# Optimization experiments

Measured on AMD Instinct MI355X. Metric: run time of the kernel, lower is better.

## Reference

```python
import jax, jax.numpy as jnp
import numpy as np

S, B, I, H = 512, 64, 1024, 1024


def setup_inputs() -> dict:
    key = jax.random.key(0)
    ks = jax.random.split(key, 17)
    sI = 1.0 / np.sqrt(I)
    sH = 1.0 / np.sqrt(H)
    d = {"x": jax.random.normal(ks[0], (S, B, I), dtype=jnp.float32)}
    names = ["i", "f", "c", "o"]
    for n, g in enumerate(names):
        d[f"w_x{g}"] = jax.random.uniform(ks[1 + 4 * n], (H, I), jnp.float32, -sI, sI)
        d[f"b_x{g}"] = jax.random.uniform(ks[2 + 4 * n], (H,), jnp.float32, -sI, sI)
        d[f"w_h{g}"] = jax.random.uniform(ks[3 + 4 * n], (H, H), jnp.float32, -sH, sH)
        d[f"b_h{g}"] = jax.random.uniform(ks[4 + 4 * n], (H,), jnp.float32, -sH, sH)
        d[f"b_{g}"] = jnp.zeros((H,), jnp.float32)
    return d


def reference(x, w_xi, b_xi, w_hi, b_hi, b_i,
              w_xf, b_xf, w_hf, b_hf, b_f,
              w_xc, b_xc, w_hc, b_hc, b_c,
              w_xo, b_xo, w_ho, b_ho, b_o):
    seq_len, batch, _ = x.shape
    hid = w_hi.shape[0]
    # Precompute all input-side projections in one big GEMM per gate: [S,B,H].
    # Fold the three bias vectors of each gate (b_x*, b_h*, b_*) in here; math
    # is identical to adding them per step.
    gx_i = jnp.einsum('sbi,hi->sbh', x, w_xi) + (b_xi + b_hi + b_i)
    gx_f = jnp.einsum('sbi,hi->sbh', x, w_xf) + (b_xf + b_hf + b_f)
    gx_c = jnp.einsum('sbi,hi->sbh', x, w_xc) + (b_xc + b_hc + b_c)
    gx_o = jnp.einsum('sbi,hi->sbh', x, w_xo) + (b_xo + b_ho + b_o)

    h0 = jnp.zeros((batch, hid), x.dtype)
    c0 = jnp.zeros((batch, hid), x.dtype)

    def step(carry, gx):
        h, c = carry
        xi, xf, xc, xo = gx
        i_t = jax.nn.sigmoid(xi + h @ w_hi.T)
        f_t = jax.nn.sigmoid(xf + h @ w_hf.T)
        g_t = jnp.tanh(xc + h @ w_hc.T)
        o_t = jax.nn.sigmoid(xo + h @ w_ho.T)
        c = f_t * c + i_t * g_t
        h = o_t * jnp.tanh(c)
        return (h, c), h

    (h, c), outputs = jax.lax.scan(step, (h0, c0), (gx_i, gx_f, gx_c, gx_o))
    return outputs, (h, c)
```

## Files before the change

kernel.cpp:

```cpp
#include <hip/hip_runtime.h>
#include <cstdint>
#include <cstddef>

#define S_LEN 512
#define NB    64
#define NI    1024
#define NH    1024
#define NR    4096
#define NGRP  4
#define WPG   64
#define BPG   16
#define HSLOT 33792
#define FLAGSTRIDE 16

typedef short bf16x8 __attribute__((ext_vector_type(8)));
typedef float f32x4  __attribute__((ext_vector_type(4)));

__device__ __forceinline__ short f2bf(float f) {
  uint32_t u = __float_as_uint(f);
  u += 0x7fff + ((u >> 16) & 1);
  return (short)(u >> 16);
}
__device__ __forceinline__ float bf2f(short s) {
  return __uint_as_float(((uint32_t)(uint16_t)s) << 16);
}
__device__ __forceinline__ void gload16(const void* g, void* l) {
  __builtin_amdgcn_global_load_lds((const __attribute__((address_space(1))) void*)g,
                                   (__attribute__((address_space(3))) void*)l, 16, 0, 0);
}
__device__ __forceinline__ float sigm(float x) { return 1.0f / (1.0f + __expf(-x)); }
__device__ __forceinline__ float tanh_fast(float x) {
  return 2.0f / (1.0f + __expf(-2.0f * x)) - 1.0f;
}

__device__ __forceinline__ void astore32(void* p, uint32_t v) {
  __hip_atomic_store((uint32_t*)p, v, __ATOMIC_RELAXED, __HIP_MEMORY_SCOPE_AGENT);
}
__device__ __forceinline__ uint32_t aload32(const void* p) {
  return __hip_atomic_load((const uint32_t*)p, __ATOMIC_RELAXED, __HIP_MEMORY_SCOPE_AGENT);
}


__global__ __launch_bounds__(256) void k_convert_x(const float* __restrict__ x,
                                                   short* __restrict__ xbf) {
  int tid = blockIdx.x * 256 + threadIdx.x;
  float4 v = ((const float4*)x)[tid];
  short4 o;
  o.x = f2bf(v.x); o.y = f2bf(v.y); o.z = f2bf(v.z); o.w = f2bf(v.w);
  ((short4*)xbf)[tid] = o;
}

struct WPtrs { const float *xi, *xf, *xc, *xo, *hi, *hf, *hc, *ho; };

__global__ __launch_bounds__(256) void k_pack_w(WPtrs w, short* __restrict__ wxcat,
                                                short* __restrict__ whcat) {
  int tid  = blockIdx.x * 256 + threadIdx.x;
  int flat = tid * 4;
  int r = flat >> 10, k = flat & 1023;
  int j = r >> 2, g = r & 3;
  const float* px = (g == 0) ? w.xi : (g == 1) ? w.xf : (g == 2) ? w.xc : w.xo;
  const float* ph = (g == 0) ? w.hi : (g == 1) ? w.hf : (g == 2) ? w.hc : w.ho;
  float4 vx = *(const float4*)(px + j * 1024 + k);
  float4 vh = *(const float4*)(ph + j * 1024 + k);
  short4 ox, oh;
  ox.x = f2bf(vx.x); ox.y = f2bf(vx.y); ox.z = f2bf(vx.z); ox.w = f2bf(vx.w);
  oh.x = f2bf(vh.x); oh.y = f2bf(vh.y); oh.z = f2bf(vh.z); oh.w = f2bf(vh.w);
  *(short4*)(wxcat + flat) = ox;
  *(short4*)(whcat + flat) = oh;
}

struct BPtrs { const float *xi,*hi,*i_, *xf,*hf,*f_, *xc,*hc,*c_, *xo,*ho,*o_; };

__global__ __launch_bounds__(256) void k_init(BPtrs p, float* __restrict__ bias,
                                              unsigned int* __restrict__ flags) {
  int tid = blockIdx.x * 256 + threadIdx.x;
  flags[tid] = 0;
  int j = tid >> 2, g = tid & 3;
  const float* bx = (g == 0) ? p.xi : (g == 1) ? p.xf : (g == 2) ? p.xc : p.xo;
  const float* bh = (g == 0) ? p.hi : (g == 1) ? p.hf : (g == 2) ? p.hc : p.ho;
  const float* bb = (g == 0) ? p.i_ : (g == 1) ? p.f_ : (g == 2) ? p.c_ : p.o_;
  bias[tid] = bx[j] + bh[j] + bb[j];
}


__global__ __launch_bounds__(256) void gemm_x(const short* __restrict__ xbf,
                                              const short* __restrict__ wx,
                                              const float* __restrict__ bias,
                                              short* __restrict__ gx) {
  __shared__ __align__(16) short As[2][4096];
  __shared__ __align__(16) short Bs[2][4096];

  const int tid = threadIdx.x, wave = tid >> 6, lane = tid & 63;
  const int m0 = blockIdx.x * 128, n0 = blockIdx.y * 128;
  const char* aB = (const char*)xbf + (size_t)m0 * 2048;
  const char* bB = (const char*)wx + (size_t)n0 * 2048;

  f32x4 acc[4][4] = {};

  auto stage = [&](int kt, int buf) {
#pragma unroll
    for (int s2 = 0; s2 < 2; ++s2) {
      int seg = wave * 2 + s2;
      int L   = seg * 1024 + lane * 16;
      int row = L >> 6;
      int cb  = L & 63;
      gload16(aB + (size_t)row * 2048 + kt * 64 + cb, (char*)&As[buf][0] + L);
      gload16(bB + (size_t)row * 2048 + kt * 64 + cb, (char*)&Bs[buf][0] + L);
    }
  };

  const int wm = wave >> 1, wn = wave & 1;
  auto compute = [&](int buf) {
    const char* Ab = (const char*)&As[buf][0];
    const char* Bb = (const char*)&Bs[buf][0];
    bf16x8 a[4], b[4];
#pragma unroll
    for (int f = 0; f < 4; ++f) {
      int ar = wm * 64 + f * 16 + (lane & 15);
      a[f] = *(const bf16x8*)(Ab + ar * 64 + (lane >> 4) * 16);
      int br = wn * 64 + f * 16 + (lane & 15);
      b[f] = *(const bf16x8*)(Bb + br * 64 + (lane >> 4) * 16);
    }
#pragma unroll
    for (int i = 0; i < 4; ++i)
#pragma unroll
      for (int j = 0; j < 4; ++j)
        acc[i][j] = __builtin_amdgcn_mfma_f32_16x16x32_bf16(a[i], b[j], acc[i][j], 0, 0, 0);
  };

  stage(0, 0);
  __syncthreads();
  int buf = 0;
  for (int kt = 0; kt < 32; ++kt) {
    if (kt < 31) stage(kt + 1, buf ^ 1);
    compute(buf);
    __syncthreads();
    buf ^= 1;
  }

  const int colL = lane & 15;
#pragma unroll
  for (int j = 0; j < 4; ++j) {
    int   n  = n0 + wn * 64 + j * 16 + colL;
    float bv = bias[n];
#pragma unroll
    for (int i = 0; i < 4; ++i) {
#pragma unroll
      for (int q = 0; q < 4; ++q) {
        int m = m0 + wm * 64 + i * 16 + (lane >> 4) * 4 + q;
        __builtin_nontemporal_store((short)f2bf(acc[i][j][q] + bv),
                                    &gx[(size_t)m * NR + n]);
      }
    }
  }
}

#define LDS_BYTES (131072 + 2 * 16 * 65 * 4)

__global__ __launch_bounds__(256, 1) void lstm_persist(
    const short* __restrict__ gx,
    const short* __restrict__ wh,
    char* __restrict__ hb,
    unsigned int* __restrict__ flags,
    float* __restrict__ out) {
  extern __shared__ __align__(16) char lds[];
  char* WhC = lds;
  float (*pre)[16][65] = (float(*)[16][65])(lds + 131072);

  const int tid = threadIdx.x, wave = tid >> 6, lane = tid & 63;
  const int grp = blockIdx.x & 3;
  const int wq  = blockIdx.x >> 2;
  const int r0  = wq * 64;
  const int j0  = wq * 16;
  const char* whB = (const char*)(wh + (size_t)r0 * NH);
  char* hb_g = hb + (size_t)grp * S_LEN * HSLOT;
  unsigned int* flags_g = flags + grp * WPG * FLAGSTRIDE;

#pragma unroll
  for (int p = 0; p < 32; ++p) {
    int L = p * 4096 + tid * 16;
    int row = L >> 11, kb = L & 2047;
    gload16(whB + (size_t)row * 2048 + (kb ^ ((row & 7) << 4)), lds + L);
  }

  const int b_pw = tid >> 3;
  const int jp   = tid & 7;
  float c_reg[2] = {0.f, 0.f};

  const int aoff = (lane >> 5) * 512 + (lane & 15) * 32 + ((lane >> 4) & 1) * 16;
  const int br   = wave * 16 + (lane & 15);
  const int bswz = (br & 7) << 4;
  const int bcol = (lane >> 4) * 16;

  const unsigned int* fpoll = flags_g + lane * FLAGSTRIDE;

  const short* gx_me = gx + ((size_t)grp * BPG + b_pw) * NR + j0 * 4 + jp * 8;

  __syncthreads();

  bf16x8 gx_cur = {}, gx_nxt = {};
  if (tid < 128) gx_cur = *(const bf16x8*)(gx_me);

  for (int t = 0; t < S_LEN; ++t) {
    f32x4 acc0 = {}, acc1 = {};
    if (t) {
      const char* hs = hb_g + (size_t)(t - 1) * HSLOT + aoff;
      bf16x8 a[32];
#pragma unroll
      for (int ks = 0; ks < 32; ++ks)
        a[ks] = *(const bf16x8*)(hs + ks * 1024);
      __builtin_amdgcn_sched_barrier(0);
#pragma unroll
      for (int ks = 0; ks < 32; ++ks) {
        int wb = ks * 64 + bcol;
        bf16x8 b0 = *(const bf16x8*)(WhC + br * 2048 + (wb ^ bswz));
        if (ks & 1) acc1 = __builtin_amdgcn_mfma_f32_16x16x32_bf16(a[ks], b0, acc1, 0, 0, 0);
        else        acc0 = __builtin_amdgcn_mfma_f32_16x16x32_bf16(a[ks], b0, acc0, 0, 0, 0);
      }
    }

    const int par = t & 1;
    {
      f32x4 a0 = acc0 + acc1;
      const int colL = lane & 15;
      const int mB   = (lane >> 4) * 4;
#pragma unroll
      for (int q = 0; q < 4; ++q)
        pre[par][mB + q][wave * 16 + colL] = a0[q];
    }
    __syncthreads();

    float hn2[2] = {0.f, 0.f};
    if (tid < 128) {
#pragma unroll
      for (int it = 0; it < 2; ++it) {
        int rl = (jp * 2 + it) * 4;
        float vi = pre[par][b_pw][rl + 0] + bf2f(gx_cur[it * 4 + 0]);
        float vf = pre[par][b_pw][rl + 1] + bf2f(gx_cur[it * 4 + 1]);
        float vg = pre[par][b_pw][rl + 2] + bf2f(gx_cur[it * 4 + 2]);
        float vo = pre[par][b_pw][rl + 3] + bf2f(gx_cur[it * 4 + 3]);
        float ig = sigm(vi), fg = sigm(vf), gg = tanh_fast(vg), og = sigm(vo);
        c_reg[it] = fg * c_reg[it] + ig * gg;
        hn2[it]   = og * tanh_fast(c_reg[it]);
      }
      if (t != S_LEN - 1) {
        char* hw = hb_g + (size_t)t * HSLOT + wq * 512 + b_pw * 32 + jp * 4;
        uint32_t hbits = (uint32_t)(uint16_t)f2bf(hn2[0]) |
                         ((uint32_t)(uint16_t)f2bf(hn2[1]) << 16);
        astore32(hw, hbits);
      }
    }

    if (t != S_LEN - 1) {
      __syncthreads();
      const unsigned want = (unsigned)(t + 1);
      if (tid == 0) astore32((void*)(flags_g + wq * FLAGSTRIDE), want);
    }

    if (tid < 128) {
      float2 of = { hn2[0], hn2[1] };
      *(float2*)(out + ((size_t)t * NB + grp * BPG + b_pw) * NH + j0 + jp * 2) = of;
      if (t == S_LEN - 1) {
        float* oh = out + (size_t)S_LEN * NB * NH;
        int ci = (grp * BPG + b_pw) * NH + j0 + jp * 2;
        *(float2*)(oh + ci) = of;
        float2 cf = { c_reg[0], c_reg[1] };
        *(float2*)(oh + NB * NH + ci) = cf;
      }
    }

    if (t != S_LEN - 1) {
      if (tid < 128) {
        const int tp = (t + 1 < S_LEN) ? t + 1 : t;
        gx_nxt = *(const bf16x8*)(gx_me + (size_t)tp * NB * NR);
      }
      const unsigned want = (unsigned)(t + 1);
      if (wave == 0) {
        uint32_t v = aload32(fpoll);
        while (!__all(v >= want)) {
          __builtin_amdgcn_s_sleep(1);
          v = aload32(fpoll);
        }
      }
      __syncthreads();
      gx_cur = gx_nxt;
    }
  }
}


extern "C" void kernel_launch(void* const* d_in, const int* in_sizes, int n_in,
                              void* d_out, int out_size, void* d_ws, size_t ws_size,
                              hipStream_t stream) {
  const float* x   = (const float*)d_in[0];
  const float* wxi = (const float*)d_in[1];
  const float* bxi = (const float*)d_in[2];
  const float* whi = (const float*)d_in[3];
  const float* bhi = (const float*)d_in[4];
  const float* bi  = (const float*)d_in[5];
  const float* wxf = (const float*)d_in[6];
  const float* bxf = (const float*)d_in[7];
  const float* whf = (const float*)d_in[8];
  const float* bhf = (const float*)d_in[9];
  const float* bf  = (const float*)d_in[10];
  const float* wxc = (const float*)d_in[11];
  const float* bxc = (const float*)d_in[12];
  const float* whc = (const float*)d_in[13];
  const float* bhc = (const float*)d_in[14];
  const float* bc  = (const float*)d_in[15];
  const float* wxo = (const float*)d_in[16];
  const float* bxo = (const float*)d_in[17];
  const float* who = (const float*)d_in[18];
  const float* bho = (const float*)d_in[19];
  const float* bo  = (const float*)d_in[20];

  char* ws = (char*)d_ws;
  const size_t SB = (size_t)S_LEN * NB;
  size_t off = 0;
  short* gxp   = (short*)(ws + off); off += SB * NR * 2;
  short* xbf   = (short*)(ws + off); off += SB * NI * 2;
  short* wxcat = (short*)(ws + off); off += (size_t)NR * NI * 2;
  short* whcat = (short*)(ws + off); off += (size_t)NR * NH * 2;
  float* bias  = (float*)(ws + off); off += NR * 4;
  unsigned int* flags = (unsigned int*)(ws + off); off += NGRP * WPG * FLAGSTRIDE * 4;
  (void)ws_size; (void)in_sizes; (void)n_in; (void)out_size;

  char* hb = (char*)xbf;

  float* out = (float*)d_out;

  (void)hipFuncSetAttribute((const void*)lstm_persist,
                            hipFuncAttributeMaxDynamicSharedMemorySize, LDS_BYTES);

  k_convert_x<<<(int)(SB * NI / 4 / 256), 256, 0, stream>>>(x, xbf);
  WPtrs wp = {wxi, wxf, wxc, wxo, whi, whf, whc, who};
  k_pack_w<<<(NR * NI / 4) / 256, 256, 0, stream>>>(wp, wxcat, whcat);
  BPtrs bp = {bxi, bhi, bi, bxf, bhf, bf, bxc, bhc, bc, bxo, bho, bo};
  k_init<<<NR / 256, 256, 0, stream>>>(bp, bias, flags);

  gemm_x<<<dim3(SB / 128, NR / 128), 256, 0, stream>>>(xbf, wxcat, bias, gxp);

  lstm_persist<<<NGRP * WPG, 256, LDS_BYTES, stream>>>(gxp, whcat, hb, flags, out);
}
```

Before: 2.194 ms.

## Swap MFMA operands so gate math runs directly on accumulators without LDS

Swaps the A/B operands of the recurrent MFMA so each lane's accumulator holds the four gates (i,f,g,o) of one hidden unit for one batch row. The gate nonlinearities and cell update then run in registers on all 256 threads, which removes the LDS staging buffer and one block barrier per timestep. The gx prefetch for the next step is also moved ahead of the MFMA loop to hide its latency. In exchange, h is written with 16-bit atomic stores and out with scalar 4-byte stores, both less coalesced than before.

```diff
diff --git a/kernel.cpp b/kernel.cpp
--- a/kernel.cpp
+++ b/kernel.cpp
@@ -35,6 +35,9 @@
 
 __device__ __forceinline__ void astore32(void* p, uint32_t v) {
   __hip_atomic_store((uint32_t*)p, v, __ATOMIC_RELAXED, __HIP_MEMORY_SCOPE_AGENT);
+}
+__device__ __forceinline__ void astore16(void* p, uint16_t v) {
+  __hip_atomic_store((uint16_t*)p, v, __ATOMIC_RELAXED, __HIP_MEMORY_SCOPE_AGENT);
 }
 __device__ __forceinline__ uint32_t aload32(const void* p) {
   return __hip_atomic_load((const uint32_t*)p, __ATOMIC_RELAXED, __HIP_MEMORY_SCOPE_AGENT);
@@ -155,7 +158,7 @@
   }
 }
 
-#define LDS_BYTES (131072 + 2 * 16 * 65 * 4)
+#define LDS_BYTES 131072
 
 __global__ __launch_bounds__(256, 1) void lstm_persist(
     const short* __restrict__ gx,
@@ -165,7 +168,6 @@
     float* __restrict__ out) {
   extern __shared__ __align__(16) char lds[];
   char* WhC = lds;
-  float (*pre)[16][65] = (float(*)[16][65])(lds + 131072);
 
   const int tid = threadIdx.x, wave = tid >> 6, lane = tid & 63;
   const int grp = blockIdx.x & 3;
@@ -183,9 +185,9 @@
     gload16(whB + (size_t)row * 2048 + (kb ^ ((row & 7) << 4)), lds + L);
   }
 
-  const int b_pw = tid >> 3;
-  const int jp   = tid & 7;
-  float c_reg[2] = {0.f, 0.f};
+  const int b_ln = lane & 15;
+  const int jl   = wave * 4 + (lane >> 4);
+  float c_reg = 0.f;
 
   const int aoff = (lane >> 5) * 512 + (lane & 15) * 32 + ((lane >> 4) & 1) * 16;
   const int br   = wave * 16 + (lane & 15);
@@ -194,12 +196,14 @@
 
   const unsigned int* fpoll = flags_g + lane * FLAGSTRIDE;
 
-  const short* gx_me = gx + ((size_t)grp * BPG + b_pw) * NR + j0 * 4 + jp * 8;
+  const short* gx_me = gx + ((size_t)grp * BPG + b_ln) * NR + (j0 + jl) * 4;
+  char* h_me = hb_g + wq * 512 + b_ln * 32 + jl * 2;
+  float* out_me = out + (size_t)(grp * BPG + b_ln) * NH + j0 + jl;
 
   __syncthreads();
 
-  bf16x8 gx_cur = {}, gx_nxt = {};
-  if (tid < 128) gx_cur = *(const bf16x8*)(gx_me);
+  short4 gx_cur = *(const short4*)(gx_me);
+  short4 gx_nxt;
 
   for (int t = 0; t < S_LEN; ++t) {
     f32x4 acc0 = {}, acc1 = {};
@@ -209,72 +213,45 @@
 #pragma unroll
       for (int ks = 0; ks < 32; ++ks)
         a[ks] = *(const bf16x8*)(hs + ks * 1024);
+      {
+        const int tp = (t + 1 < S_LEN) ? t + 1 : t;
+        gx_nxt = *(const short4*)(gx_me + (size_t)tp * NB * NR);
+      }
       __builtin_amdgcn_sched_barrier(0);
 #pragma unroll
       for (int ks = 0; ks < 32; ++ks) {
         int wb = ks * 64 + bcol;
-        bf16x8 b0 = *(const bf16x8*)(WhC + br * 2048 + (wb ^ bswz));
-        if (ks & 1) acc1 = __builtin_amdgcn_mfma_f32_16x16x32_bf16(a[ks], b0, acc1, 0, 0, 0);
-        else        acc0 = __builtin_amdgcn_mfma_f32_16x16x32_bf16(a[ks], b0, acc0, 0, 0, 0);
+        bf16x8 w0 = *(const bf16x8*)(WhC + br * 2048 + (wb ^ bswz));
+        if (ks & 1) acc1 = __builtin_amdgcn_mfma_f32_16x16x32_bf16(w0, a[ks], acc1, 0, 0, 0);
+        else        acc0 = __builtin_amdgcn_mfma_f32_16x16x32_bf16(w0, a[ks], acc0, 0, 0, 0);
       }
-    }
-
-    const int par = t & 1;
-    {
-      f32x4 a0 = acc0 + acc1;
-      const int colL = lane & 15;
-      const int mB   = (lane >> 4) * 4;
-#pragma unroll
-      for (int q = 0; q < 4; ++q)
-        pre[par][mB + q][wave * 16 + colL] = a0[q];
-    }
-    __syncthreads();
-
-    float hn2[2] = {0.f, 0.f};
-    if (tid < 128) {
-#pragma unroll
-      for (int it = 0; it < 2; ++it) {
-        int rl = (jp * 2 + it) * 4;
-        float vi = pre[par][b_pw][rl + 0] + bf2f(gx_cur[it * 4 + 0]);
-        float vf = pre[par][b_pw][rl + 1] + bf2f(gx_cur[it * 4 + 1]);
-        float vg = pre[par][b_pw][rl + 2] + bf2f(gx_cur[it * 4 + 2]);
-        float vo = pre[par][b_pw][rl + 3] + bf2f(gx_cur[it * 4 + 3]);
-        float ig = sigm(vi), fg = sigm(vf), gg = tanh_fast(vg), og = sigm(vo);
-        c_reg[it] = fg * c_reg[it] + ig * gg;
-        hn2[it]   = og * tanh_fast(c_reg[it]);
-      }
-      if (t != S_LEN - 1) {
-        char* hw = hb_g + (size_t)t * HSLOT + wq * 512 + b_pw * 32 + jp * 4;
-        uint32_t hbits = (uint32_t)(uint16_t)f2bf(hn2[0]) |
-                         ((uint32_t)(uint16_t)f2bf(hn2[1]) << 16);
-        astore32(hw, hbits);
-      }
+    } else {
+      gx_nxt = *(const short4*)(gx_me + (size_t)NB * NR);
+    }
+
+    f32x4 a0 = acc0 + acc1;
+    float vi = a0[0] + bf2f(gx_cur.x);
+    float vf = a0[1] + bf2f(gx_cur.y);
+    float vg = a0[2] + bf2f(gx_cur.z);
+    float vo = a0[3] + bf2f(gx_cur.w);
+    float ig = sigm(vi), fg = sigm(vf), gg = tanh_fast(vg), og = sigm(vo);
+    c_reg = fg * c_reg + ig * gg;
+    float hn = og * tanh_fast(c_reg);
+
+    if (t != S_LEN - 1)
+      astore16(h_me + (size_t)t * HSLOT, (uint16_t)(uint16_t)f2bf(hn));
+    out_me[(size_t)t * NB * NH] = hn;
+    if (t == S_LEN - 1) {
+      float* oh = out + (size_t)S_LEN * NB * NH;
+      size_t ci = (size_t)(grp * BPG + b_ln) * NH + j0 + jl;
+      oh[ci] = hn;
+      oh[(size_t)NB * NH + ci] = c_reg;
     }
 
     if (t != S_LEN - 1) {
       __syncthreads();
       const unsigned want = (unsigned)(t + 1);
       if (tid == 0) astore32((void*)(flags_g + wq * FLAGSTRIDE), want);
-    }
-
-    if (tid < 128) {
-      float2 of = { hn2[0], hn2[1] };
-      *(float2*)(out + ((size_t)t * NB + grp * BPG + b_pw) * NH + j0 + jp * 2) = of;
-      if (t == S_LEN - 1) {
-        float* oh = out + (size_t)S_LEN * NB * NH;
-        int ci = (grp * BPG + b_pw) * NH + j0 + jp * 2;
-        *(float2*)(oh + ci) = of;
-        float2 cf = { c_reg[0], c_reg[1] };
-        *(float2*)(oh + NB * NH + ci) = cf;
-      }
-    }
-
-    if (t != S_LEN - 1) {
-      if (tid < 128) {
-        const int tp = (t + 1 < S_LEN) ? t + 1 : t;
-        gx_nxt = *(const bf16x8*)(gx_me + (size_t)tp * NB * NR);
-      }
-      const unsigned want = (unsigned)(t + 1);
       if (wave == 0) {
         uint32_t v = aload32(fpoll);
         while (!__all(v >= want)) {
```

Result: slower. 2.246 ms (+2.4%).

## Enlarge input GEMM tiles to 256x256 with swizzled LDS and explicit pipelining

Applied to the files above, without the earlier changes.

Rewrites the input-projection GEMM to use 256x256 output tiles per 512-thread workgroup with 128 KB of dynamic LDS. K-chunks are 128 wide and double-buffered. LDS rows are XOR-swizzled to avoid bank conflicts, and block IDs are remapped so neighbouring workgroups share operand tiles in cache. Explicit vmcnt waits, s_barriers and setprio control how loads overlap with MFMA work. The aim is higher arithmetic intensity and MFMA utilisation, at the cost of one workgroup per CU and heavier register pressure from the 8x4 accumulator array.

```diff
diff --git a/kernel.cpp b/kernel.cpp
--- a/kernel.cpp
+++ b/kernel.cpp
@@ -82,73 +82,98 @@
   bias[tid] = bx[j] + bh[j] + bb[j];
 }
 
-
-__global__ __launch_bounds__(256) void gemm_x(const short* __restrict__ xbf,
-                                              const short* __restrict__ wx,
-                                              const float* __restrict__ bias,
-                                              short* __restrict__ gx) {
-  __shared__ __align__(16) short As[2][4096];
-  __shared__ __align__(16) short Bs[2][4096];
+#define GX_LDS 131072
+
+__global__ __launch_bounds__(512, 1) void gemm_x(const short* __restrict__ xbf,
+                                                 const short* __restrict__ wx,
+                                                 const float* __restrict__ bias,
+                                                 short* __restrict__ gx) {
+  extern __shared__ __align__(16) char lds[];
 
   const int tid = threadIdx.x, wave = tid >> 6, lane = tid & 63;
-  const int m0 = blockIdx.x * 128, n0 = blockIdx.y * 128;
+  const int wm = wave >> 2, wn = wave & 3;
+
+  const int bid = blockIdx.x;
+  const int wg  = (bid & 7) * 256 + (bid >> 3);
+  const int nt  = wg >> 7, mt = wg & 127;
+  const int m0  = mt * 256, n0 = nt * 256;
   const char* aB = (const char*)xbf + (size_t)m0 * 2048;
   const char* bB = (const char*)wx + (size_t)n0 * 2048;
 
-  f32x4 acc[4][4] = {};
-
-  auto stage = [&](int kt, int buf) {
-#pragma unroll
-    for (int s2 = 0; s2 < 2; ++s2) {
-      int seg = wave * 2 + s2;
-      int L   = seg * 1024 + lane * 16;
-      int row = L >> 6;
-      int cb  = L & 63;
-      gload16(aB + (size_t)row * 2048 + kt * 64 + cb, (char*)&As[buf][0] + L);
-      gload16(bB + (size_t)row * 2048 + kt * 64 + cb, (char*)&Bs[buf][0] + L);
+  auto stage = [&](int buf, int kt) {
+#pragma unroll
+    for (int s2 = 0; s2 < 4; ++s2) {
+      const int   op   = s2 >> 1, half = s2 & 1;
+      const char* src0 = op ? bB : aB;
+      char*       dst0 = lds + op * 65536 + buf * 32768 + half * 16384;
+#pragma unroll
+      for (int ss = 0; ss < 2; ++ss) {
+        int L = ss * 8192 + tid * 16;
+        int r128 = L >> 7, cb = L & 127;
+        gload16(src0 + (size_t)(half * 128 + r128) * 2048 + kt * 128
+                     + (cb ^ ((r128 & 7) << 4)),
+                dst0 + L);
+      }
     }
   };
 
-  const int wm = wave >> 1, wn = wave & 1;
-  auto compute = [&](int buf) {
-    const char* Ab = (const char*)&As[buf][0];
-    const char* Bb = (const char*)&Bs[buf][0];
-    bf16x8 a[4], b[4];
-#pragma unroll
-    for (int f = 0; f < 4; ++f) {
-      int ar = wm * 64 + f * 16 + (lane & 15);
-      a[f] = *(const bf16x8*)(Ab + ar * 64 + (lane >> 4) * 16);
-      int br = wn * 64 + f * 16 + (lane & 15);
-      b[f] = *(const bf16x8*)(Bb + br * 64 + (lane >> 4) * 16);
-    }
-#pragma unroll
-    for (int i = 0; i < 4; ++i)
-#pragma unroll
-      for (int j = 0; j < 4; ++j)
-        acc[i][j] = __builtin_amdgcn_mfma_f32_16x16x32_bf16(a[i], b[j], acc[i][j], 0, 0, 0);
-  };
+  f32x4 acc[8][4] = {};
+  const int colL = lane & 15;
+  const int kchk = (lane >> 4) * 16;
 
   stage(0, 0);
-  __syncthreads();
   int buf = 0;
-  for (int kt = 0; kt < 32; ++kt) {
-    if (kt < 31) stage(kt + 1, buf ^ 1);
-    compute(buf);
-    __syncthreads();
+  for (int kt = 0; kt < 16; ++kt) {
+    if (kt < 15) stage(buf ^ 1, kt + 1);
+    __builtin_amdgcn_sched_barrier(0);
+    if (kt < 15) asm volatile("s_waitcnt vmcnt(8)" ::: "memory");
+    else         asm volatile("s_waitcnt vmcnt(0)" ::: "memory");
+    __builtin_amdgcn_s_barrier();
+    __builtin_amdgcn_sched_barrier(0);
+
+    const char* Ab = lds + buf * 32768 + wm * 16384;
+    const char* Bb = lds + 65536 + buf * 32768;
+    __builtin_amdgcn_s_setprio(1);
+#pragma unroll
+    for (int kk = 0; kk < 2; ++kk) {
+      bf16x8 b[4], a[8];
+#pragma unroll
+      for (int jn = 0; jn < 4; ++jn) {
+        int row = wn * 64 + jn * 16 + colL;
+        int r128 = row & 127;
+        b[jn] = *(const bf16x8*)(Bb + (row >> 7) * 16384 + r128 * 128
+                                 + ((kk * 64 + kchk) ^ ((r128 & 7) << 4)));
+      }
+#pragma unroll
+      for (int i = 0; i < 8; ++i) {
+        int r128 = i * 16 + colL;
+        a[i] = *(const bf16x8*)(Ab + r128 * 128
+                                + ((kk * 64 + kchk) ^ ((r128 & 7) << 4)));
+      }
+#pragma unroll
+      for (int i = 0; i < 8; ++i)
+#pragma unroll
+        for (int jn = 0; jn < 4; ++jn)
+          acc[i][jn] = __builtin_amdgcn_mfma_f32_16x16x32_bf16(a[i], b[jn], acc[i][jn], 0, 0, 0);
+    }
+    __builtin_amdgcn_s_setprio(0);
+    __builtin_amdgcn_sched_barrier(0);
+    asm volatile("s_waitcnt lgkmcnt(0)" ::: "memory");
+    __builtin_amdgcn_s_barrier();
+    __builtin_amdgcn_sched_barrier(0);
     buf ^= 1;
   }
 
-  const int colL = lane & 15;
-#pragma unroll
-  for (int j = 0; j < 4; ++j) {
-    int   n  = n0 + wn * 64 + j * 16 + colL;
+#pragma unroll
+  for (int jn = 0; jn < 4; ++jn) {
+    int   n  = n0 + wn * 64 + jn * 16 + colL;
     float bv = bias[n];
 #pragma unroll
-    for (int i = 0; i < 4; ++i) {
+    for (int i = 0; i < 8; ++i) {
 #pragma unroll
       for (int q = 0; q < 4; ++q) {
-        int m = m0 + wm * 64 + i * 16 + (lane >> 4) * 4 + q;
-        __builtin_nontemporal_store((short)f2bf(acc[i][j][q] + bv),
+        int m = m0 + wm * 128 + i * 16 + (lane >> 4) * 4 + q;
+        __builtin_nontemporal_store((short)f2bf(acc[i][jn][q] + bv),
                                     &gx[(size_t)m * NR + n]);
       }
     }
@@ -331,6 +356,8 @@
 
   (void)hipFuncSetAttribute((const void*)lstm_persist,
                             hipFuncAttributeMaxDynamicSharedMemorySize, LDS_BYTES);
+  (void)hipFuncSetAttribute((const void*)gemm_x,
+                            hipFuncAttributeMaxDynamicSharedMemorySize, GX_LDS);
 
   k_convert_x<<<(int)(SB * NI / 4 / 256), 256, 0, stream>>>(x, xbf);
   WPtrs wp = {wxi, wxf, wxc, wxo, whi, whf, whc, who};
@@ -338,7 +365,7 @@
   BPtrs bp = {bxi, bhi, bi, bxf, bhf, bf, bxc, bhc, bc, bxo, bho, bo};
   k_init<<<NR / 256, 256, 0, stream>>>(bp, bias, flags);
 
-  gemm_x<<<dim3(SB / 128, NR / 128), 256, 0, stream>>>(xbf, wxcat, bias, gxp);
+  gemm_x<<<(SB / 256) * (NR / 256), 512, GX_LDS, stream>>>(xbf, wxcat, bias, gxp);
 
   lstm_persist<<<NGRP * WPG, 256, LDS_BYTES, stream>>>(gxp, whcat, hb, flags, out);
 }
```

Result: faster. 2.011 ms (-8.3%).
